# Optimization experiments

Measured on AMD Instinct MI355X. Metric: run time of the kernel, lower is better.

The kernel has to match this reference:

```python
import jax, jax.numpy as jnp
import numpy as np

LAMBDA_TEMPORAL = 0.5
LAMBDA_IDENTITY = 0.1
EPS = 1e-6


def setup_inputs() -> dict:
    key = jax.random.key(0)
    k1, k2, k3 = jax.random.split(key, 3)
    B, T, N = 16, 256, 2048
    pred_tracks_3d = jax.random.normal(k1, (B, T, N, 3), dtype=jnp.float32)
    gt_tracks_3d = jax.random.normal(k2, (B, T, N, 3), dtype=jnp.float32)
    gt_visibility = jax.random.uniform(k3, (B, T, N), dtype=jnp.float32)
    return {
        'pred_tracks_3d': pred_tracks_3d,
        'gt_tracks_3d': gt_tracks_3d,
        'gt_visibility': gt_visibility,
    }


def _compute_losses(pred, gt, vis):
    # visibility mask (B, T, N)
    m = (vis > 0.5).astype(pred.dtype)
    num_visible = jnp.sum(m)

    coord_w = jnp.array([1.0, 1.0, 2.0], dtype=pred.dtype)
    weighted_sq = jnp.square(pred - gt) * coord_w  # (B,T,N,3)
    recon = jnp.where(
        num_visible > 0,
        jnp.sum(weighted_sq * m[..., None]) / jnp.maximum(num_visible, 1.0),
        0.0,
    )

    # --- temporal: masked velocity MSE (visible in both adjacent frames) ---
    pred_vel = pred[:, 1:] - pred[:, :-1]
    gt_vel = gt[:, 1:] - gt[:, :-1]
    vel_mask = m[:, 1:] * m[:, :-1]  # (B,T-1,N)
    num_vel = jnp.sum(vel_mask)
    temporal = jnp.where(
        num_vel > 0,
        jnp.sum(jnp.square(pred_vel - gt_vel) * vel_mask[..., None]) / jnp.maximum(num_vel, 1.0),
        0.0,
    )

    # --- identity: per-point unbiased variance ratio over visible (b,t) samples ---
    n = jnp.sum(m, axis=(0, 1))  # (N,) visible count per point

    def masked_var(x):
        # unbiased (ddof=1) per-point, per-coord variance over masked (B,T) entries
        mean = jnp.einsum('btn,btnc->nc', m, x) / jnp.maximum(n, 1.0)[:, None]
        ss = jnp.einsum('btn,btnc->nc', m, jnp.square(x - mean[None, None]))
        return ss / jnp.maximum(n - 1.0, 1.0)[:, None]  # (N,3)

    pred_var = masked_var(pred)
    gt_var = masked_var(gt)
    var_ratio = jnp.sum(jnp.abs(pred_var - gt_var), axis=1) / (jnp.sum(gt_var, axis=1) + EPS)
    num_points = pred.shape[2]
    identity = jnp.sum(jnp.where(n > 1, var_ratio, 0.0)) / num_points

    # --- adaptive re-weighting (no-grad in original) ---
    rl = jax.lax.stop_gradient(recon)
    tl = jax.lax.stop_gradient(temporal)
    il = jax.lax.stop_gradient(identity)
    all_pos = (rl > 0) & (tl > 0) & (il > 0)
    max_comp = jnp.maximum(jnp.maximum(rl, tl), il)
    target = max_comp / 3.0
    thresh = 10.0 * target

    def adjust(base, comp):
        return jnp.where(all_pos & (comp > thresh), base * target / jnp.maximum(comp, 1e-30), base)

    rec_w = adjust(1.0, rl)
    temp_w = adjust(LAMBDA_TEMPORAL, tl)
    id_w = adjust(LAMBDA_IDENTITY, il)

    total = rec_w * recon + temp_w * temporal + id_w * identity
    return jnp.stack([total, recon, temporal, identity])


def reference(pred_tracks_3d, gt_tracks_3d, gt_visibility):
    # returns [total_loss, reconstruction_loss, temporal_loss, identity_loss]
    return _compute_losses(pred_tracks_3d, gt_tracks_3d, gt_visibility)
```

## Files before the change

### kernel.cpp

```cpp
#include <hip/hip_runtime.h>

#define BB 16
#define TT 256
#define NN 2048
#define TC 16
#define NSLICE 8
#define WSBASE 16


__device__ __forceinline__ float waveReduceSum(float v) {
#pragma unroll
  for (int o = 32; o > 0; o >>= 1) v += __shfl_down(v, o, 64);
  return v;
}

__global__ __launch_bounds__(256, 8) void stats_kernel(
    const float* __restrict__ pred, const float* __restrict__ gt,
    const float* __restrict__ vis, float* __restrict__ ws) {
  const int n  = blockIdx.x * 256 + threadIdx.x;
  const int b  = blockIdx.y;
  const int t0 = blockIdx.z * TC;

  const size_t frame0 = (size_t)(b * TT + t0) * NN + n;
  const float3* __restrict__ pp = (const float3*)pred + frame0;
  const float3* __restrict__ gp = (const float3*)gt + frame0;
  const float*  __restrict__ vp = vis + frame0;

  float cnt = 0.f;
  float sp0 = 0, sp1 = 0, sp2 = 0, qp0 = 0, qp1 = 0, qp2 = 0;
  float sg0 = 0, sg1 = 0, sg2 = 0, qg0 = 0, qg1 = 0, qg2 = 0;
  float recon = 0, temporal = 0, nvel = 0;

  float3 ppv, pgv;
  float mprev;
  {
    const long off = (t0 == 0) ? 0 : -(long)NN;
    ppv = pp[off];
    pgv = gp[off];
    float v = vp[off];
    mprev = (t0 != 0 && v > 0.5f) ? 1.f : 0.f;
  }

#pragma unroll
  for (int i = 0; i < TC; ++i) {
    float3 a = pp[(size_t)i * NN];
    float3 g = gp[(size_t)i * NN];
    float v = vp[(size_t)i * NN];
    float m = (v > 0.5f) ? 1.f : 0.f;

    cnt += m;
    sp0 += m * a.x; sp1 += m * a.y; sp2 += m * a.z;
    qp0 += m * a.x * a.x; qp1 += m * a.y * a.y; qp2 += m * a.z * a.z;
    sg0 += m * g.x; sg1 += m * g.y; sg2 += m * g.z;
    qg0 += m * g.x * g.x; qg1 += m * g.y * g.y; qg2 += m * g.z * g.z;
    float d0 = a.x - g.x, d1 = a.y - g.y, d2 = a.z - g.z;
    recon += m * (d0 * d0 + d1 * d1 + 2.f * d2 * d2);

    float mv = m * mprev;
    float vx = (a.x - ppv.x) - (g.x - pgv.x);
    float vy = (a.y - ppv.y) - (g.y - pgv.y);
    float vz = (a.z - ppv.z) - (g.z - pgv.z);
    temporal += mv * (vx * vx + vy * vy + vz * vz);
    nvel += mv;

    ppv = a; pgv = g; mprev = m;
  }

  float* pts = ws + WSBASE + (size_t)(b & (NSLICE - 1)) * 13 * NN;
  atomicAdd(&pts[0 * NN + n], cnt);
  atomicAdd(&pts[1 * NN + n], sp0);
  atomicAdd(&pts[2 * NN + n], sp1);
  atomicAdd(&pts[3 * NN + n], sp2);
  atomicAdd(&pts[4 * NN + n], qp0);
  atomicAdd(&pts[5 * NN + n], qp1);
  atomicAdd(&pts[6 * NN + n], qp2);
  atomicAdd(&pts[7 * NN + n], sg0);
  atomicAdd(&pts[8 * NN + n], sg1);
  atomicAdd(&pts[9 * NN + n], sg2);
  atomicAdd(&pts[10 * NN + n], qg0);
  atomicAdd(&pts[11 * NN + n], qg1);
  atomicAdd(&pts[12 * NN + n], qg2);

  __shared__ float sred[3][4];
  float r0 = waveReduceSum(recon);
  float r1 = waveReduceSum(temporal);
  float r2 = waveReduceSum(nvel);
  int lane = threadIdx.x & 63, w = threadIdx.x >> 6;
  if (lane == 0) { sred[0][w] = r0; sred[1][w] = r1; sred[2][w] = r2; }
  __syncthreads();
  if (threadIdx.x < 3) {
    float s = sred[threadIdx.x][0] + sred[threadIdx.x][1] +
              sred[threadIdx.x][2] + sred[threadIdx.x][3];
    atomicAdd(&ws[threadIdx.x], s);
  }
}

__global__ __launch_bounds__(256) void identity_kernel(float* __restrict__ ws) {
  const int n = blockIdx.x * 256 + threadIdx.x;
  const float* base = ws + WSBASE;
  float st[13];
#pragma unroll
  for (int k = 0; k < 13; ++k) st[k] = 0.f;
#pragma unroll
  for (int s = 0; s < NSLICE; ++s) {
    const float* pts = base + (size_t)s * 13 * NN;
#pragma unroll
    for (int k = 0; k < 13; ++k) st[k] += pts[k * NN + n];
  }
  float c = st[0];
  float sp0 = st[1], sp1 = st[2], sp2 = st[3];
  float qp0 = st[4], qp1 = st[5], qp2 = st[6];
  float sg0 = st[7], sg1 = st[8], sg2 = st[9];
  float qg0 = st[10], qg1 = st[11], qg2 = st[12];

  float inv = 1.f / fmaxf(c, 1.f);
  float dv  = 1.f / fmaxf(c - 1.f, 1.f);
  float pv0 = (qp0 - sp0 * sp0 * inv) * dv;
  float pv1 = (qp1 - sp1 * sp1 * inv) * dv;
  float pv2 = (qp2 - sp2 * sp2 * inv) * dv;
  float gv0 = (qg0 - sg0 * sg0 * inv) * dv;
  float gv1 = (qg1 - sg1 * sg1 * inv) * dv;
  float gv2 = (qg2 - sg2 * sg2 * inv) * dv;

  float num = fabsf(pv0 - gv0) + fabsf(pv1 - gv1) + fabsf(pv2 - gv2);
  float den = gv0 + gv1 + gv2 + 1e-6f;
  float contrib = (c > 1.f) ? (num / den) : 0.f;

  __shared__ float sred[2][4];
  float r0 = waveReduceSum(contrib);
  float r1 = waveReduceSum(c);
  int lane = threadIdx.x & 63, w = threadIdx.x >> 6;
  if (lane == 0) { sred[0][w] = r0; sred[1][w] = r1; }
  __syncthreads();
  if (threadIdx.x < 2) {
    float s = sred[threadIdx.x][0] + sred[threadIdx.x][1] +
              sred[threadIdx.x][2] + sred[threadIdx.x][3];
    atomicAdd(&ws[3 + threadIdx.x], s);
  }
}

__global__ void finalize_kernel(const float* __restrict__ ws, float* __restrict__ out) {
  float nv = ws[4];
  float recon = (nv > 0.f) ? ws[0] / fmaxf(nv, 1.f) : 0.f;
  float nvel = ws[2];
  float temporal = (nvel > 0.f) ? ws[1] / fmaxf(nvel, 1.f) : 0.f;
  float identity = ws[3] / (float)NN;

  float rl = recon, tl = temporal, il = identity;
  bool all_pos = (rl > 0.f) && (tl > 0.f) && (il > 0.f);
  float maxc = fmaxf(rl, fmaxf(tl, il));
  float target = maxc / 3.f;
  float thresh = 10.f * target;
  float rw = (all_pos && rl > thresh) ? 1.0f * target / fmaxf(rl, 1e-30f) : 1.0f;
  float tw = (all_pos && tl > thresh) ? 0.5f * target / fmaxf(tl, 1e-30f) : 0.5f;
  float iw = (all_pos && il > thresh) ? 0.1f * target / fmaxf(il, 1e-30f) : 0.1f;

  out[0] = rw * recon + tw * temporal + iw * identity;
  out[1] = recon;
  out[2] = temporal;
  out[3] = identity;
}

extern "C" void kernel_launch(void* const* d_in, const int* in_sizes, int n_in,
                              void* d_out, int out_size, void* d_ws, size_t ws_size,
                              hipStream_t stream) {
  const float* pred = (const float*)d_in[0];
  const float* gt   = (const float*)d_in[1];
  const float* vis  = (const float*)d_in[2];
  float* out = (float*)d_out;
  float* ws  = (float*)d_ws;

  hipMemsetAsync(d_ws, 0, (WSBASE + (size_t)NSLICE * 13 * NN) * sizeof(float), stream);

  dim3 g1(NN / 256, BB, TT / TC);
  stats_kernel<<<g1, 256, 0, stream>>>(pred, gt, vis, ws);
  identity_kernel<<<dim3(NN / 256), 256, 0, stream>>>(ws);
  finalize_kernel<<<1, 1, 0, stream>>>(ws, out);
}
```

Measured before the change: 254.2 us.

## Replace per-point atomics with per-slice plain stores and reduce in identity kernel

Measured after the change: 331.9 us. 1.31x slower.

```diff
diff --git a/kernel.cpp b/kernel.cpp
--- a/kernel.cpp
+++ b/kernel.cpp
@@ -4,7 +4,8 @@
 #define TT 256
 #define NN 2048
 #define TC 16
-#define NSLICE 8
+#define NSLICES (BB * (TT / TC))
+#define NSLICE_ATOMIC 8
 #define WSBASE 16
 
 
@@ -14,12 +15,14 @@
   return v;
 }
 
+template <bool USE_ATOMIC>
 __global__ __launch_bounds__(256, 8) void stats_kernel(
     const float* __restrict__ pred, const float* __restrict__ gt,
     const float* __restrict__ vis, float* __restrict__ ws) {
   const int n  = blockIdx.x * 256 + threadIdx.x;
   const int b  = blockIdx.y;
-  const int t0 = blockIdx.z * TC;
+  const int tz = blockIdx.z;
+  const int t0 = tz * TC;
 
   const size_t frame0 = (size_t)(b * TT + t0) * NN + n;
   const float3* __restrict__ pp = (const float3*)pred + frame0;
@@ -66,20 +69,18 @@
     ppv = a; pgv = g; mprev = m;
   }
 
-  float* pts = ws + WSBASE + (size_t)(b & (NSLICE - 1)) * 13 * NN;
-  atomicAdd(&pts[0 * NN + n], cnt);
-  atomicAdd(&pts[1 * NN + n], sp0);
-  atomicAdd(&pts[2 * NN + n], sp1);
-  atomicAdd(&pts[3 * NN + n], sp2);
-  atomicAdd(&pts[4 * NN + n], qp0);
-  atomicAdd(&pts[5 * NN + n], qp1);
-  atomicAdd(&pts[6 * NN + n], qp2);
-  atomicAdd(&pts[7 * NN + n], sg0);
-  atomicAdd(&pts[8 * NN + n], sg1);
-  atomicAdd(&pts[9 * NN + n], sg2);
-  atomicAdd(&pts[10 * NN + n], qg0);
-  atomicAdd(&pts[11 * NN + n], qg1);
-  atomicAdd(&pts[12 * NN + n], qg2);
+  float st[13] = {cnt, sp0, sp1, sp2, qp0, qp1, qp2,
+                  sg0, sg1, sg2, qg0, qg1, qg2};
+  if (USE_ATOMIC) {
+    float* pts = ws + WSBASE + (size_t)(b & (NSLICE_ATOMIC - 1)) * 13 * NN;
+#pragma unroll
+    for (int k = 0; k < 13; ++k) atomicAdd(&pts[k * NN + n], st[k]);
+  } else {
+    const int slice = b * (TT / TC) + tz;
+    float* pts = ws + WSBASE + (size_t)slice * 13 * NN;
+#pragma unroll
+    for (int k = 0; k < 13; ++k) pts[k * NN + n] = st[k];
+  }
 
   __shared__ float sred[3][4];
   float r0 = waveReduceSum(recon);
@@ -95,14 +96,14 @@
   }
 }
 
+template <int NSL>
 __global__ __launch_bounds__(256) void identity_kernel(float* __restrict__ ws) {
   const int n = blockIdx.x * 256 + threadIdx.x;
   const float* base = ws + WSBASE;
   float st[13];
 #pragma unroll
   for (int k = 0; k < 13; ++k) st[k] = 0.f;
-#pragma unroll
-  for (int s = 0; s < NSLICE; ++s) {
+  for (int s = 0; s < NSL; ++s) {
     const float* pts = base + (size_t)s * 13 * NN;
 #pragma unroll
     for (int k = 0; k < 13; ++k) st[k] += pts[k * NN + n];
@@ -170,10 +171,19 @@
   float* out = (float*)d_out;
   float* ws  = (float*)d_ws;
 
-  hipMemsetAsync(d_ws, 0, (WSBASE + (size_t)NSLICE * 13 * NN) * sizeof(float), stream);
+  const size_t slice_bytes = (WSBASE + (size_t)NSLICES * 13 * NN) * sizeof(float);
+  dim3 g1(NN / 256, BB, TT / TC);
 
-  dim3 g1(NN / 256, BB, TT / TC);
-  stats_kernel<<<g1, 256, 0, stream>>>(pred, gt, vis, ws);
-  identity_kernel<<<dim3(NN / 256), 256, 0, stream>>>(ws);
+  if (ws_size >= slice_bytes) {
+    hipMemsetAsync(d_ws, 0, WSBASE * sizeof(float), stream);
+    stats_kernel<false><<<g1, 256, 0, stream>>>(pred, gt, vis, ws);
+    identity_kernel<NSLICES><<<dim3(NN / 256), 256, 0, stream>>>(ws);
+  } else {
+    hipMemsetAsync(d_ws, 0,
+                   (WSBASE + (size_t)NSLICE_ATOMIC * 13 * NN) * sizeof(float),
+                   stream);
+    stats_kernel<true><<<g1, 256, 0, stream>>>(pred, gt, vis, ws);
+    identity_kernel<NSLICE_ATOMIC><<<dim3(NN / 256), 256, 0, stream>>>(ws);
+  }
   finalize_kernel<<<1, 1, 0, stream>>>(ws, out);
 }
```

## Process four points per thread with float4 loads in stats kernel

Applied to the files above, without the earlier changes.

Result: slower. 388.3 us (+52.7%).

```diff
diff --git a/kernel.cpp b/kernel.cpp
--- a/kernel.cpp
+++ b/kernel.cpp
@@ -3,7 +3,7 @@
 #define BB 16
 #define TT 256
 #define NN 2048
-#define TC 16
+#define TC 8
 #define NSLICE 8
 #define WSBASE 16
 
@@ -14,72 +14,98 @@
   return v;
 }
 
-__global__ __launch_bounds__(256, 8) void stats_kernel(
+__global__ __launch_bounds__(256) void stats_kernel(
     const float* __restrict__ pred, const float* __restrict__ gt,
     const float* __restrict__ vis, float* __restrict__ ws) {
-  const int n  = blockIdx.x * 256 + threadIdx.x;
+  const int kg = blockIdx.x * 256 + threadIdx.x;
   const int b  = blockIdx.y;
   const int t0 = blockIdx.z * TC;
 
-  const size_t frame0 = (size_t)(b * TT + t0) * NN + n;
-  const float3* __restrict__ pp = (const float3*)pred + frame0;
-  const float3* __restrict__ gp = (const float3*)gt + frame0;
-  const float*  __restrict__ vp = vis + frame0;
-
-  float cnt = 0.f;
-  float sp0 = 0, sp1 = 0, sp2 = 0, qp0 = 0, qp1 = 0, qp2 = 0;
-  float sg0 = 0, sg1 = 0, sg2 = 0, qg0 = 0, qg1 = 0, qg2 = 0;
-  float recon = 0, temporal = 0, nvel = 0;
-
-  float3 ppv, pgv;
-  float mprev;
+  const float4* __restrict__ p4 = (const float4*)pred;
+  const float4* __restrict__ g4 = (const float4*)gt;
+  const float4* __restrict__ v4 = (const float4*)vis;
+
+  const size_t f0 = (size_t)(b * TT + t0);
+  const size_t kp3 = 3 * (size_t)kg;
+
+  float st[4][13];
+#pragma unroll
+  for (int p = 0; p < 4; ++p)
+#pragma unroll
+    for (int k = 0; k < 13; ++k) st[p][k] = 0.f;
+  float recon = 0.f, temporal = 0.f, nvel = 0.f;
+
+  float pa[12], pg[12], pm[4];
   {
-    const long off = (t0 == 0) ? 0 : -(long)NN;
-    ppv = pp[off];
-    pgv = gp[off];
-    float v = vp[off];
-    mprev = (t0 != 0 && v > 0.5f) ? 1.f : 0.f;
+    const size_t fb = (t0 == 0) ? f0 : f0 - 1;
+    const size_t ip = fb * (NN * 3 / 4) + kp3;
+    const size_t iv = fb * (NN / 4) + kg;
+    float4 A0 = p4[ip], A1 = p4[ip + 1], A2 = p4[ip + 2];
+    float4 G0 = g4[ip], G1 = g4[ip + 1], G2 = g4[ip + 2];
+    float4 V = v4[iv];
+    pa[0]=A0.x; pa[1]=A0.y; pa[2]=A0.z; pa[3]=A0.w; pa[4]=A1.x; pa[5]=A1.y;
+    pa[6]=A1.z; pa[7]=A1.w; pa[8]=A2.x; pa[9]=A2.y; pa[10]=A2.z; pa[11]=A2.w;
+    pg[0]=G0.x; pg[1]=G0.y; pg[2]=G0.z; pg[3]=G0.w; pg[4]=G1.x; pg[5]=G1.y;
+    pg[6]=G1.z; pg[7]=G1.w; pg[8]=G2.x; pg[9]=G2.y; pg[10]=G2.z; pg[11]=G2.w;
+    const float z = (t0 == 0) ? 0.f : 1.f;
+    pm[0] = (V.x > 0.5f) ? z : 0.f;
+    pm[1] = (V.y > 0.5f) ? z : 0.f;
+    pm[2] = (V.z > 0.5f) ? z : 0.f;
+    pm[3] = (V.w > 0.5f) ? z : 0.f;
   }
 
 #pragma unroll
   for (int i = 0; i < TC; ++i) {
-    float3 a = pp[(size_t)i * NN];
-    float3 g = gp[(size_t)i * NN];
-    float v = vp[(size_t)i * NN];
-    float m = (v > 0.5f) ? 1.f : 0.f;
-
-    cnt += m;
-    sp0 += m * a.x; sp1 += m * a.y; sp2 += m * a.z;
-    qp0 += m * a.x * a.x; qp1 += m * a.y * a.y; qp2 += m * a.z * a.z;
-    sg0 += m * g.x; sg1 += m * g.y; sg2 += m * g.z;
-    qg0 += m * g.x * g.x; qg1 += m * g.y * g.y; qg2 += m * g.z * g.z;
-    float d0 = a.x - g.x, d1 = a.y - g.y, d2 = a.z - g.z;
-    recon += m * (d0 * d0 + d1 * d1 + 2.f * d2 * d2);
-
-    float mv = m * mprev;
-    float vx = (a.x - ppv.x) - (g.x - pgv.x);
-    float vy = (a.y - ppv.y) - (g.y - pgv.y);
-    float vz = (a.z - ppv.z) - (g.z - pgv.z);
-    temporal += mv * (vx * vx + vy * vy + vz * vz);
-    nvel += mv;
-
-    ppv = a; pgv = g; mprev = m;
+    const size_t f = f0 + i;
+    const size_t ip = f * (NN * 3 / 4) + kp3;
+    const size_t iv = f * (NN / 4) + kg;
+    float4 A0 = p4[ip], A1 = p4[ip + 1], A2 = p4[ip + 2];
+    float4 G0 = g4[ip], G1 = g4[ip + 1], G2 = g4[ip + 2];
+    float4 V = v4[iv];
+
+    float ca[12], cg[12], cm[4];
+    ca[0]=A0.x; ca[1]=A0.y; ca[2]=A0.z; ca[3]=A0.w; ca[4]=A1.x; ca[5]=A1.y;
+    ca[6]=A1.z; ca[7]=A1.w; ca[8]=A2.x; ca[9]=A2.y; ca[10]=A2.z; ca[11]=A2.w;
+    cg[0]=G0.x; cg[1]=G0.y; cg[2]=G0.z; cg[3]=G0.w; cg[4]=G1.x; cg[5]=G1.y;
+    cg[6]=G1.z; cg[7]=G1.w; cg[8]=G2.x; cg[9]=G2.y; cg[10]=G2.z; cg[11]=G2.w;
+    cm[0] = (V.x > 0.5f) ? 1.f : 0.f;
+    cm[1] = (V.y > 0.5f) ? 1.f : 0.f;
+    cm[2] = (V.z > 0.5f) ? 1.f : 0.f;
+    cm[3] = (V.w > 0.5f) ? 1.f : 0.f;
+
+#pragma unroll
+    for (int p = 0; p < 4; ++p) {
+      const float m = cm[p];
+      const float ax = ca[3*p], ay = ca[3*p+1], az = ca[3*p+2];
+      const float gx = cg[3*p], gy = cg[3*p+1], gz = cg[3*p+2];
+      st[p][0] += m;
+      st[p][1] += m * ax;      st[p][2] += m * ay;      st[p][3] += m * az;
+      st[p][4] += m * ax * ax; st[p][5] += m * ay * ay; st[p][6] += m * az * az;
+      st[p][7] += m * gx;      st[p][8] += m * gy;      st[p][9] += m * gz;
+      st[p][10] += m * gx * gx; st[p][11] += m * gy * gy; st[p][12] += m * gz * gz;
+      const float d0 = ax - gx, d1 = ay - gy, d2 = az - gz;
+      recon += m * (d0 * d0 + d1 * d1 + 2.f * d2 * d2);
+
+      const float mv = m * pm[p];
+      const float vx = (ax - pa[3*p])   - (gx - pg[3*p]);
+      const float vy = (ay - pa[3*p+1]) - (gy - pg[3*p+1]);
+      const float vz = (az - pa[3*p+2]) - (gz - pg[3*p+2]);
+      temporal += mv * (vx * vx + vy * vy + vz * vz);
+      nvel += mv;
+    }
+#pragma unroll
+    for (int j = 0; j < 12; ++j) { pa[j] = ca[j]; pg[j] = cg[j]; }
+#pragma unroll
+    for (int p = 0; p < 4; ++p) pm[p] = cm[p];
   }
 
   float* pts = ws + WSBASE + (size_t)(b & (NSLICE - 1)) * 13 * NN;
-  atomicAdd(&pts[0 * NN + n], cnt);
-  atomicAdd(&pts[1 * NN + n], sp0);
-  atomicAdd(&pts[2 * NN + n], sp1);
-  atomicAdd(&pts[3 * NN + n], sp2);
-  atomicAdd(&pts[4 * NN + n], qp0);
-  atomicAdd(&pts[5 * NN + n], qp1);
-  atomicAdd(&pts[6 * NN + n], qp2);
-  atomicAdd(&pts[7 * NN + n], sg0);
-  atomicAdd(&pts[8 * NN + n], sg1);
-  atomicAdd(&pts[9 * NN + n], sg2);
-  atomicAdd(&pts[10 * NN + n], qg0);
-  atomicAdd(&pts[11 * NN + n], qg1);
-  atomicAdd(&pts[12 * NN + n], qg2);
+  const int n0 = kg * 4;
+#pragma unroll
+  for (int k = 0; k < 13; ++k)
+#pragma unroll
+    for (int p = 0; p < 4; ++p)
+      atomicAdd(&pts[k * NN + n0 + p], st[p][k]);
 
   __shared__ float sred[3][4];
   float r0 = waveReduceSum(recon);
@@ -172,7 +198,7 @@
 
   hipMemsetAsync(d_ws, 0, (WSBASE + (size_t)NSLICE * 13 * NN) * sizeof(float), stream);
 
-  dim3 g1(NN / 256, BB, TT / TC);
+  dim3 g1(NN / 1024, BB, TT / TC);
   stats_kernel<<<g1, 256, 0, stream>>>(pred, gt, vis, ws);
   identity_kernel<<<dim3(NN / 256), 256, 0, stream>>>(ws);
   finalize_kernel<<<1, 1, 0, stream>>>(ws, out);
```

## Process two points per thread with float2 loads and 1024-thread blocks

Applied to the files above, without the earlier changes.

Measured after the change: 295.0 us. +16.0%, slower.

```diff
diff --git a/kernel.cpp b/kernel.cpp
--- a/kernel.cpp
+++ b/kernel.cpp
@@ -14,74 +14,99 @@
   return v;
 }
 
-__global__ __launch_bounds__(256, 8) void stats_kernel(
+__global__ __launch_bounds__(1024) void stats_kernel(
     const float* __restrict__ pred, const float* __restrict__ gt,
     const float* __restrict__ vis, float* __restrict__ ws) {
-  const int n  = blockIdx.x * 256 + threadIdx.x;
+  const int i  = threadIdx.x;
   const int b  = blockIdx.y;
-  const int t0 = blockIdx.z * TC;
-
-  const size_t frame0 = (size_t)(b * TT + t0) * NN + n;
-  const float3* __restrict__ pp = (const float3*)pred + frame0;
-  const float3* __restrict__ gp = (const float3*)gt + frame0;
-  const float*  __restrict__ vp = vis + frame0;
-
-  float cnt = 0.f;
-  float sp0 = 0, sp1 = 0, sp2 = 0, qp0 = 0, qp1 = 0, qp2 = 0;
-  float sg0 = 0, sg1 = 0, sg2 = 0, qg0 = 0, qg1 = 0, qg2 = 0;
-  float recon = 0, temporal = 0, nvel = 0;
-
-  float3 ppv, pgv;
-  float mprev;
+  const int tz = blockIdx.z;
+  const int t0 = tz * TC;
+
+  const float2* __restrict__ p2 = (const float2*)pred;
+  const float2* __restrict__ g2 = (const float2*)gt;
+  const float2* __restrict__ v2 = (const float2*)vis;
+
+  const size_t f0 = (size_t)(b * TT + t0);
+  const size_t i3 = 3 * (size_t)i;
+
+  float st0[13], st1[13];
+#pragma unroll
+  for (int k = 0; k < 13; ++k) { st0[k] = 0.f; st1[k] = 0.f; }
+  float recon = 0.f, temporal = 0.f, nvel = 0.f;
+
+  float pa0, pa1, pa2, pb0, pb1, pb2;
+  float qa0, qa1, qa2, qb0, qb1, qb2;
+  float pm0, pm1;
   {
-    const long off = (t0 == 0) ? 0 : -(long)NN;
-    ppv = pp[off];
-    pgv = gp[off];
-    float v = vp[off];
-    mprev = (t0 != 0 && v > 0.5f) ? 1.f : 0.f;
-  }
-
-#pragma unroll
-  for (int i = 0; i < TC; ++i) {
-    float3 a = pp[(size_t)i * NN];
-    float3 g = gp[(size_t)i * NN];
-    float v = vp[(size_t)i * NN];
-    float m = (v > 0.5f) ? 1.f : 0.f;
-
-    cnt += m;
-    sp0 += m * a.x; sp1 += m * a.y; sp2 += m * a.z;
-    qp0 += m * a.x * a.x; qp1 += m * a.y * a.y; qp2 += m * a.z * a.z;
-    sg0 += m * g.x; sg1 += m * g.y; sg2 += m * g.z;
-    qg0 += m * g.x * g.x; qg1 += m * g.y * g.y; qg2 += m * g.z * g.z;
-    float d0 = a.x - g.x, d1 = a.y - g.y, d2 = a.z - g.z;
-    recon += m * (d0 * d0 + d1 * d1 + 2.f * d2 * d2);
-
-    float mv = m * mprev;
-    float vx = (a.x - ppv.x) - (g.x - pgv.x);
-    float vy = (a.y - ppv.y) - (g.y - pgv.y);
-    float vz = (a.z - ppv.z) - (g.z - pgv.z);
-    temporal += mv * (vx * vx + vy * vy + vz * vz);
-    nvel += mv;
-
-    ppv = a; pgv = g; mprev = m;
-  }
-
-  float* pts = ws + WSBASE + (size_t)(b & (NSLICE - 1)) * 13 * NN;
-  atomicAdd(&pts[0 * NN + n], cnt);
-  atomicAdd(&pts[1 * NN + n], sp0);
-  atomicAdd(&pts[2 * NN + n], sp1);
-  atomicAdd(&pts[3 * NN + n], sp2);
-  atomicAdd(&pts[4 * NN + n], qp0);
-  atomicAdd(&pts[5 * NN + n], qp1);
-  atomicAdd(&pts[6 * NN + n], qp2);
-  atomicAdd(&pts[7 * NN + n], sg0);
-  atomicAdd(&pts[8 * NN + n], sg1);
-  atomicAdd(&pts[9 * NN + n], sg2);
-  atomicAdd(&pts[10 * NN + n], qg0);
-  atomicAdd(&pts[11 * NN + n], qg1);
-  atomicAdd(&pts[12 * NN + n], qg2);
-
-  __shared__ float sred[3][4];
+    const size_t fb = (t0 == 0) ? f0 : f0 - 1;
+    float2 A0 = p2[fb * 3072 + i3], A1 = p2[fb * 3072 + i3 + 1], A2 = p2[fb * 3072 + i3 + 2];
+    float2 G0 = g2[fb * 3072 + i3], G1 = g2[fb * 3072 + i3 + 1], G2 = g2[fb * 3072 + i3 + 2];
+    float2 V  = v2[fb * 1024 + i];
+    pa0 = A0.x; pa1 = A0.y; pa2 = A1.x;  pb0 = A1.y; pb1 = A2.x; pb2 = A2.y;
+    qa0 = G0.x; qa1 = G0.y; qa2 = G1.x;  qb0 = G1.y; qb1 = G2.x; qb2 = G2.y;
+    const float z = (t0 == 0) ? 0.f : 1.f;
+    pm0 = (V.x > 0.5f) ? z : 0.f;
+    pm1 = (V.y > 0.5f) ? z : 0.f;
+  }
+
+#pragma unroll
+  for (int t = 0; t < TC; ++t) {
+    const size_t f = f0 + t;
+    float2 A0 = p2[f * 3072 + i3], A1 = p2[f * 3072 + i3 + 1], A2 = p2[f * 3072 + i3 + 2];
+    float2 G0 = g2[f * 3072 + i3], G1 = g2[f * 3072 + i3 + 1], G2 = g2[f * 3072 + i3 + 2];
+    float2 V  = v2[f * 1024 + i];
+
+    const float a00 = A0.x, a01 = A0.y, a02 = A1.x;
+    const float a10 = A1.y, a11 = A2.x, a12 = A2.y;
+    const float g00 = G0.x, g01 = G0.y, g02 = G1.x;
+    const float g10 = G1.y, g11 = G2.x, g12 = G2.y;
+    const float m0 = (V.x > 0.5f) ? 1.f : 0.f;
+    const float m1 = (V.y > 0.5f) ? 1.f : 0.f;
+
+    st0[0] += m0;
+    st0[1] += m0 * a00;       st0[2] += m0 * a01;       st0[3] += m0 * a02;
+    st0[4] += m0 * a00 * a00; st0[5] += m0 * a01 * a01; st0[6] += m0 * a02 * a02;
+    st0[7] += m0 * g00;       st0[8] += m0 * g01;       st0[9] += m0 * g02;
+    st0[10] += m0 * g00 * g00; st0[11] += m0 * g01 * g01; st0[12] += m0 * g02 * g02;
+    {
+      const float d0 = a00 - g00, d1 = a01 - g01, d2 = a02 - g02;
+      recon += m0 * (d0 * d0 + d1 * d1 + 2.f * d2 * d2);
+      const float mv = m0 * pm0;
+      const float vx = (a00 - pa0) - (g00 - qa0);
+      const float vy = (a01 - pa1) - (g01 - qa1);
+      const float vz = (a02 - pa2) - (g02 - qa2);
+      temporal += mv * (vx * vx + vy * vy + vz * vz);
+      nvel += mv;
+    }
+    st1[0] += m1;
+    st1[1] += m1 * a10;       st1[2] += m1 * a11;       st1[3] += m1 * a12;
+    st1[4] += m1 * a10 * a10; st1[5] += m1 * a11 * a11; st1[6] += m1 * a12 * a12;
+    st1[7] += m1 * g10;       st1[8] += m1 * g11;       st1[9] += m1 * g12;
+    st1[10] += m1 * g10 * g10; st1[11] += m1 * g11 * g11; st1[12] += m1 * g12 * g12;
+    {
+      const float d0 = a10 - g10, d1 = a11 - g11, d2 = a12 - g12;
+      recon += m1 * (d0 * d0 + d1 * d1 + 2.f * d2 * d2);
+      const float mv = m1 * pm1;
+      const float vx = (a10 - pb0) - (g10 - qb0);
+      const float vy = (a11 - pb1) - (g11 - qb1);
+      const float vz = (a12 - pb2) - (g12 - qb2);
+      temporal += mv * (vx * vx + vy * vy + vz * vz);
+      nvel += mv;
+    }
+
+    pa0 = a00; pa1 = a01; pa2 = a02; pb0 = a10; pb1 = a11; pb2 = a12;
+    qa0 = g00; qa1 = g01; qa2 = g02; qb0 = g10; qb1 = g11; qb2 = g12;
+    pm0 = m0; pm1 = m1;
+  }
+
+  float* pts = ws + WSBASE + (size_t)((b * (TT / TC) + tz) & (NSLICE - 1)) * 13 * NN;
+  const int n0 = 2 * i;
+#pragma unroll
+  for (int k = 0; k < 13; ++k) atomicAdd(&pts[k * NN + n0], st0[k]);
+#pragma unroll
+  for (int k = 0; k < 13; ++k) atomicAdd(&pts[k * NN + n0 + 1], st1[k]);
+
+  __shared__ float sred[3][16];
   float r0 = waveReduceSum(recon);
   float r1 = waveReduceSum(temporal);
   float r2 = waveReduceSum(nvel);
@@ -89,8 +114,9 @@
   if (lane == 0) { sred[0][w] = r0; sred[1][w] = r1; sred[2][w] = r2; }
   __syncthreads();
   if (threadIdx.x < 3) {
-    float s = sred[threadIdx.x][0] + sred[threadIdx.x][1] +
-              sred[threadIdx.x][2] + sred[threadIdx.x][3];
+    float s = 0.f;
+#pragma unroll
+    for (int j = 0; j < 16; ++j) s += sred[threadIdx.x][j];
     atomicAdd(&ws[threadIdx.x], s);
   }
 }
@@ -172,8 +198,8 @@
 
   hipMemsetAsync(d_ws, 0, (WSBASE + (size_t)NSLICE * 13 * NN) * sizeof(float), stream);
 
-  dim3 g1(NN / 256, BB, TT / TC);
-  stats_kernel<<<g1, 256, 0, stream>>>(pred, gt, vis, ws);
+  dim3 g1(1, BB, TT / TC);
+  stats_kernel<<<g1, 1024, 0, stream>>>(pred, gt, vis, ws);
   identity_kernel<<<dim3(NN / 256), 256, 0, stream>>>(ws);
   finalize_kernel<<<1, 1, 0, stream>>>(ws, out);
 }
```
